# Optimization experiments

Hardware: AMD Instinct MI355X
Metric: run time of the kernel (lower is better)

The kernel has to match this reference:

```python
import jax, jax.numpy as jnp
import numpy as np

N = 100000      # nodes
E = 1000000     # edges
H_DIM = 124     # node embedding dim
CLS_DIM = 4     # node class-logit dim (H_DIM + CLS_DIM = in_features = 128)
POLAR_DIM = 2   # edge_pred_features
HIDDEN = 256
OUT = 2
LN_EPS = 1e-5


def setup_inputs() -> dict:
    key = jax.random.key(0)
    ks = jax.random.split(key, 10)
    in_dim = 2 * (H_DIM + CLS_DIM) + POLAR_DIM  # 258
    return {
        "h": jax.random.normal(ks[0], (N, H_DIM), dtype=jnp.float32),
        "cls": jax.random.normal(ks[1], (N, CLS_DIM), dtype=jnp.float32),
        "polar": jax.random.normal(ks[2], (E, POLAR_DIM), dtype=jnp.float32),
        "src": jax.random.randint(ks[3], (E,), 0, N, dtype=jnp.int64),
        "dst": jax.random.randint(ks[4], (E,), 0, N, dtype=jnp.int64),
        # parameters (PyTorch Linear default-ish init scale)
        "W1": jax.random.normal(ks[5], (in_dim, HIDDEN), dtype=jnp.float32) * (1.0 / np.sqrt(in_dim)),
        "b1": jnp.zeros((HIDDEN,), dtype=jnp.float32),
        "gamma": jnp.ones((HIDDEN,), dtype=jnp.float32),
        "beta": jnp.zeros((HIDDEN,), dtype=jnp.float32),
        "W2": jax.random.normal(ks[6], (HIDDEN, OUT), dtype=jnp.float32) * (1.0 / np.sqrt(HIDDEN)),
        "b2": jnp.zeros((OUT,), dtype=jnp.float32),
    }


def reference(h, cls, polar, src, dst, W1, b1, gamma, beta, W2, b2):
    # softmax over class logits per node (same math as softmax on gathered
    # edge copies, but computed once per node)
    cls_sm = jax.nn.softmax(cls, axis=1)                  # [N, CLS_DIM]
    # gather src/dst node features along edges
    x = jnp.concatenate(
        [h[src], cls_sm[src], polar, h[dst], cls_sm[dst]], axis=1
    )                                                     # [E, 258]
    z = x @ W1 + b1                                        # [E, HIDDEN]
    # LayerNorm
    mu = jnp.mean(z, axis=-1, keepdims=True)
    var = jnp.mean(jnp.square(z - mu), axis=-1, keepdims=True)
    z = (z - mu) * jax.lax.rsqrt(var + LN_EPS) * gamma + beta
    z = jax.nn.relu(z)
    # dropout is identity in eval mode
    score = z @ W2 + b2                                    # [E, OUT]
    return score
```

## Files before the change

### kernel.cpp

```cpp
#include <hip/hip_runtime.h>
#include <hip/hip_bf16.h>

#define NN 100000
#define EE 1000000
#define H_DIM 124
#define PCOLS 512
#define LDK 136
#define CW 132

typedef float f32x4 __attribute__((ext_vector_type(4)));
typedef short bf16x8 __attribute__((ext_vector_type(8)));
typedef _Float16 h2 __attribute__((ext_vector_type(2)));

__device__ __forceinline__ unsigned short f2bf(float f) {
    unsigned int x = __float_as_uint(f);
    unsigned int r = (x + 0x7FFFu + ((x >> 16) & 1u)) >> 16;
    return (unsigned short)r;
}
__device__ __forceinline__ unsigned int pk2bf(float a, float b) {
    return (unsigned int)f2bf(a) | ((unsigned int)f2bf(b) << 16);
}
__device__ __forceinline__ unsigned int pk2h(float a, float b) {
    h2 v = (h2){(_Float16)a, (_Float16)b};
    return __builtin_bit_cast(unsigned int, v);
}

__device__ __forceinline__ float fdot2(h2 a, h2 b, float c) {
#if __has_builtin(__builtin_amdgcn_fdot2)
    return __builtin_amdgcn_fdot2(a, b, c, false);
#else
    return c + (float)a[0] * (float)b[0] + (float)a[1] * (float)b[1];
#endif
}

struct alignas(16) H8 { h2 p[4]; };

__global__ __launch_bounds__(256) void build_w1t(const float* __restrict__ W1,
                                                 unsigned short* __restrict__ W1T) {
    int t2 = blockIdx.x * 256 + threadIdx.x;
    int j = t2 >> 7, k = t2 & 127;
    int row = (j < 256) ? k : (130 + k);
    int col = (j < 256) ? j : (j - 256);
    W1T[t2] = f2bf(W1[row * 256 + col]);
}

__global__ __launch_bounds__(256) void p_gemm(const float* __restrict__ h,
                                              const float* __restrict__ cls,
                                              const unsigned short* __restrict__ W1T,
                                              _Float16* __restrict__ P) {
    __shared__ alignas(16) unsigned short As[64 * LDK];
    __shared__ alignas(16) unsigned short Bs[128 * LDK];
    float* Cs = (float*)&Bs[0];
    const int m0 = blockIdx.x * 64;
    const int t = threadIdx.x;

    #pragma unroll
    for (int it = 0; it < 4; ++it) {
        int chunk = t + it * 256;
        int r = chunk >> 4, c8 = chunk & 15;
        int row = m0 + r;
        unsigned int w0 = 0, w1 = 0, w2 = 0, w3 = 0;
        if (row < NN) {
            if (c8 < 15) {
                const float* hp = h + (size_t)row * H_DIM + c8 * 8;
                float4 v0 = *(const float4*)(hp);
                float4 v1 = *(const float4*)(hp + 4);
                w0 = pk2bf(v0.x, v0.y); w1 = pk2bf(v0.z, v0.w);
                w2 = pk2bf(v1.x, v1.y); w3 = pk2bf(v1.z, v1.w);
            } else {
                float4 v0 = *(const float4*)(h + (size_t)row * H_DIM + 120);
                float4 c = *(const float4*)(cls + (size_t)row * 4);
                float m = fmaxf(fmaxf(c.x, c.y), fmaxf(c.z, c.w));
                float e0 = __expf(c.x - m), e1 = __expf(c.y - m);
                float e2 = __expf(c.z - m), e3 = __expf(c.w - m);
                float inv = 1.0f / (e0 + e1 + e2 + e3);
                w0 = pk2bf(v0.x, v0.y); w1 = pk2bf(v0.z, v0.w);
                w2 = pk2bf(e0 * inv, e1 * inv); w3 = pk2bf(e2 * inv, e3 * inv);
            }
        }
        *(uint4*)(&As[r * LDK + c8 * 8]) = make_uint4(w0, w1, w2, w3);
    }
    __syncthreads();

    const int wave = t >> 6, lane = t & 63;
    const int wm = wave & 1, wn = wave >> 1;
    const int lm = lane & 15, quad = lane >> 4;

    bf16x8 afrag[4][2];
    #pragma unroll
    for (int s = 0; s < 4; ++s) {
        int k0 = s * 32 + quad * 8;
        #pragma unroll
        for (int mt = 0; mt < 2; ++mt)
            afrag[s][mt] = *(const bf16x8*)(&As[(wm * 32 + mt * 16 + lm) * LDK + k0]);
    }

    for (int cchunk = 0; cchunk < 4; ++cchunk) {
        const int n0 = cchunk * 128;
        if (cchunk) __syncthreads();
        #pragma unroll
        for (int it = 0; it < 8; ++it) {
            int chunk = t + it * 256;
            int r = chunk >> 4, c = chunk & 15;
            float4 v = *(const float4*)(W1T + (n0 + r) * 128 + c * 8);
            *(float4*)(&Bs[r * LDK + c * 8]) = v;
        }
        __syncthreads();

        f32x4 acc[2][4];
        #pragma unroll
        for (int mt = 0; mt < 2; ++mt)
            #pragma unroll
            for (int nt = 0; nt < 4; ++nt)
                acc[mt][nt] = (f32x4){0.f, 0.f, 0.f, 0.f};

        #pragma unroll
        for (int s = 0; s < 4; ++s) {
            int k0 = s * 32 + quad * 8;
            bf16x8 b[4];
            #pragma unroll
            for (int nt = 0; nt < 4; ++nt)
                b[nt] = *(const bf16x8*)(&Bs[(wn * 64 + nt * 16 + lm) * LDK + k0]);
            #pragma unroll
            for (int mt = 0; mt < 2; ++mt)
                #pragma unroll
                for (int nt = 0; nt < 4; ++nt)
                    acc[mt][nt] = __builtin_amdgcn_mfma_f32_16x16x32_bf16(afrag[s][mt], b[nt], acc[mt][nt], 0, 0, 0);
        }
        __syncthreads();

        #pragma unroll
        for (int mt = 0; mt < 2; ++mt)
            #pragma unroll
            for (int nt = 0; nt < 4; ++nt) {
                int col = wn * 64 + nt * 16 + lm;
                int rb  = wm * 32 + mt * 16 + quad * 4;
                #pragma unroll
                for (int r = 0; r < 4; ++r)
                    Cs[(rb + r) * CW + col] = acc[mt][nt][r];
            }
        __syncthreads();

        #pragma unroll
        for (int it = 0; it < 4; ++it) {
            int chunk = t + it * 256;
            int r = chunk >> 4, c8 = chunk & 15;
            float4 a = *(const float4*)(Cs + r * CW + c8 * 8);
            float4 b = *(const float4*)(Cs + r * CW + c8 * 8 + 4);
            uint4 o = make_uint4(pk2h(a.x, a.y), pk2h(a.z, a.w),
                                 pk2h(b.x, b.y), pk2h(b.z, b.w));
            int row = m0 + r;
            if (row < NN)
                *(uint4*)(P + (size_t)row * PCOLS + n0 + c8 * 8) = o;
        }
    }
}

#define K3_BLOCKS 2048
#define K3_WAVES (K3_BLOCKS * 4)

__global__ __launch_bounds__(256) void edge_kernel(const _Float16* __restrict__ P,
                                                   const int* __restrict__ src,
                                                   const int* __restrict__ dst,
                                                   const float* __restrict__ polar,
                                                   const float* __restrict__ W1,
                                                   const float* __restrict__ b1,
                                                   const float* __restrict__ gamma,
                                                   const float* __restrict__ beta,
                                                   const float* __restrict__ W2,
                                                   const float* __restrict__ b2,
                                                   float* __restrict__ out) {
    const int lane = threadIdx.x & 63;
    const int il   = lane & 31;
    const int half = lane >> 5;
    const int wid  = blockIdx.x * 4 + (threadIdx.x >> 6);
    const int jb   = il * 8;

    h2 w0c[4], w1c[4], b1c[4], gc[4], bc[4], w2ac[4], w2bc[4];
    #pragma unroll
    for (int p = 0; p < 4; ++p) {
        int j = jb + 2 * p;
        float2 a0 = *(const float2*)(W1 + 128 * 256 + j);
        float2 a1 = *(const float2*)(W1 + 129 * 256 + j);
        float2 ab = *(const float2*)(b1 + j);
        float2 ag = *(const float2*)(gamma + j);
        float2 ae = *(const float2*)(beta + j);
        float4 w2v = *(const float4*)(W2 + 2 * j);
        w0c[p]  = (h2){(_Float16)a0.x, (_Float16)a0.y};
        w1c[p]  = (h2){(_Float16)a1.x, (_Float16)a1.y};
        b1c[p]  = (h2){(_Float16)ab.x, (_Float16)ab.y};
        gc[p]   = (h2){(_Float16)ag.x, (_Float16)ag.y};
        bc[p]   = (h2){(_Float16)ae.x, (_Float16)ae.y};
        w2ac[p] = (h2){(_Float16)w2v.x, (_Float16)w2v.z};
        w2bc[p] = (h2){(_Float16)w2v.y, (_Float16)w2v.w};
    }
    const float b20 = b2[0], b21 = b2[1];
    const h2 onep = (h2){(_Float16)1.0f, (_Float16)1.0f};
    const h2 zerop = (h2){(_Float16)0.0f, (_Float16)0.0f};

    const int stride = K3_WAVES * 2;
    const int base = wid * 2;

    int s0, d0, s1, d1;
    float q00, q01, q10, q11;
    {
        int b = base, e = (b < EE) ? (b + half) : 0;
        s0 = src[e]; d0 = dst[e];
        float2 pw = *(const float2*)(polar + 2 * e);
        q00 = pw.x; q01 = pw.y;
    }
    {
        int b = base + stride, e = (b < EE) ? (b + half) : 0;
        s1 = src[e]; d1 = dst[e];
        float2 pw = *(const float2*)(polar + 2 * e);
        q10 = pw.x; q11 = pw.y;
    }
    H8 ps = *(const H8*)(P + (size_t)s0 * PCOLS + jb);
    H8 pd = *(const H8*)(P + (size_t)d0 * PCOLS + 256 + jb);

    for (int e = base; e < EE; e += stride) {
        int s2, d2; float q20, q21;
        {
            int b = e + 2 * stride, ec = (b < EE) ? (b + half) : 0;
            s2 = src[ec]; d2 = dst[ec];
            float2 pw = *(const float2*)(polar + 2 * ec);
            q20 = pw.x; q21 = pw.y;
        }
        H8 psn = *(const H8*)(P + (size_t)s1 * PCOLS + jb);
        H8 pdn = *(const H8*)(P + (size_t)d1 * PCOLS + 256 + jb);

        h2 p0h = (h2){(_Float16)q00, (_Float16)q00};
        h2 p1h = (h2){(_Float16)q01, (_Float16)q01};
        h2 z[4];
        float sum = 0.f, ss = 0.f;
        #pragma unroll
        for (int p = 0; p < 4; ++p) {
            h2 c = w0c[p] * p0h + (w1c[p] * p1h + b1c[p]);
            z[p] = (ps.p[p] + pd.p[p]) + c;
            sum = fdot2(z[p], onep, sum);
            ss  = fdot2(z[p], z[p], ss);
        }
        #pragma unroll
        for (int off = 16; off; off >>= 1) {
            sum += __shfl_xor(sum, off);
            ss  += __shfl_xor(ss, off);
        }
        float mu   = sum * (1.0f / 256.0f);
        float var  = ss * (1.0f / 256.0f) - mu * mu;
        float rstd = rsqrtf(var + 1e-5f);
        h2 muh = (h2){(_Float16)mu, (_Float16)mu};
        h2 rsh = (h2){(_Float16)rstd, (_Float16)rstd};

        float o0 = 0.f, o1 = 0.f;
        #pragma unroll
        for (int p = 0; p < 4; ++p) {
            h2 t = (z[p] - muh) * rsh;
            h2 u = t * gc[p] + bc[p];
            u = __builtin_elementwise_max(u, zerop);
            o0 = fdot2(u, w2ac[p], o0);
            o1 = fdot2(u, w2bc[p], o1);
        }
        #pragma unroll
        for (int off = 16; off; off >>= 1) {
            o0 += __shfl_xor(o0, off);
            o1 += __shfl_xor(o1, off);
        }
        if (il == 0) {
            *(float2*)(out + 2 * (e + half)) = make_float2(o0 + b20, o1 + b21);
        }

        s0 = s1; d0 = d1; q00 = q10; q01 = q11;
        s1 = s2; d1 = d2; q10 = q20; q11 = q21;
        ps = psn; pd = pdn;
    }
}

extern "C" void kernel_launch(void* const* d_in, const int* in_sizes, int n_in,
                              void* d_out, int out_size, void* d_ws, size_t ws_size,
                              hipStream_t stream) {
    const float* h     = (const float*)d_in[0];
    const float* cls   = (const float*)d_in[1];
    const float* polar = (const float*)d_in[2];
    const int*   src   = (const int*)d_in[3];
    const int*   dst   = (const int*)d_in[4];
    const float* W1    = (const float*)d_in[5];
    const float* b1    = (const float*)d_in[6];
    const float* gamma = (const float*)d_in[7];
    const float* beta  = (const float*)d_in[8];
    const float* W2    = (const float*)d_in[9];
    const float* b2    = (const float*)d_in[10];
    float* out = (float*)d_out;

    char* ws = (char*)d_ws;
    _Float16*       P   = (_Float16*)ws;
    unsigned short* W1T = (unsigned short*)(ws + 102400000);

    build_w1t<<<256, 256, 0, stream>>>(W1, W1T);

    p_gemm<<<1563, 256, 0, stream>>>(h, cls, W1T, P);

    edge_kernel<<<K3_BLOCKS, 256, 0, stream>>>(P, src, dst, polar, W1, b1, gamma, beta, W2, b2, out);
}
```

Baseline: 303.1 us.

## Process four edges per wave with 16-lane groups, DPP reductions, fold b1 into P

The edge kernel now gives each edge 16 lanes with 16 hidden columns apiece, so a wave handles four edges at once instead of two. Each wave runs a fixed 16-round fully unrolled loop over a doubled grid, double-buffering the index and P gathers. The cross-lane sums for LayerNorm and the output dot product use DPP row operations in place of shuffles. Bias b1 is added once per node in the P GEMM epilogue rather than per edge. This cuts shuffle latency and per-edge arithmetic and gives wider per-lane loads, at the cost of more registers per lane and a launch geometry hard-coded to cover exactly E edges.

```diff
diff --git a/kernel.cpp b/kernel.cpp
--- a/kernel.cpp
+++ b/kernel.cpp
@@ -32,6 +32,28 @@
     return c + (float)a[0] * (float)b[0] + (float)a[1] * (float)b[1];
 #endif
 }
+
+#if __has_builtin(__builtin_amdgcn_update_dpp)
+template <int CTRL>
+__device__ __forceinline__ float dpp_add(float x) {
+    int xi = __builtin_bit_cast(int, x);
+    int t = __builtin_amdgcn_update_dpp(xi, xi, CTRL, 0xF, 0xF, false);
+    return x + __builtin_bit_cast(float, t);
+}
+__device__ __forceinline__ float reduce16(float x) {
+    x = dpp_add<0x128>(x);
+    x = dpp_add<0x124>(x);
+    x = dpp_add<0x122>(x);
+    x = dpp_add<0x121>(x);
+    return x;
+}
+#else
+__device__ __forceinline__ float reduce16(float x) {
+    x += __shfl_xor(x, 8); x += __shfl_xor(x, 4);
+    x += __shfl_xor(x, 2); x += __shfl_xor(x, 1);
+    return x;
+}
+#endif
 
 struct alignas(16) H8 { h2 p[4]; };
 
@@ -47,6 +69,7 @@
 __global__ __launch_bounds__(256) void p_gemm(const float* __restrict__ h,
                                               const float* __restrict__ cls,
                                               const unsigned short* __restrict__ W1T,
+                                              const float* __restrict__ b1,
                                               _Float16* __restrict__ P) {
     __shared__ alignas(16) unsigned short As[64 * LDK];
     __shared__ alignas(16) unsigned short Bs[128 * LDK];
@@ -147,6 +170,13 @@
             int r = chunk >> 4, c8 = chunk & 15;
             float4 a = *(const float4*)(Cs + r * CW + c8 * 8);
             float4 b = *(const float4*)(Cs + r * CW + c8 * 8 + 4);
+            if (n0 >= 256) {
+                int cb = n0 + c8 * 8 - 256;
+                float4 ba = *(const float4*)(b1 + cb);
+                float4 bb = *(const float4*)(b1 + cb + 4);
+                a.x += ba.x; a.y += ba.y; a.z += ba.z; a.w += ba.w;
+                b.x += bb.x; b.y += bb.y; b.z += bb.z; b.w += bb.w;
+            }
             uint4 o = make_uint4(pk2h(a.x, a.y), pk2h(a.z, a.w),
                                  pk2h(b.x, b.y), pk2h(b.z, b.w));
             int row = m0 + r;
@@ -156,123 +186,126 @@
     }
 }
 
-#define K3_BLOCKS 2048
-#define K3_WAVES (K3_BLOCKS * 4)
+#define K3_BLOCKS 4096
+#define K3_WAVES  (K3_BLOCKS * 4)
+#define K3_STRIDE (K3_WAVES * 4)
+#define K3_ROUNDS 16
+
+struct EIdx { int s, d; float q0, q1; };
+
+__device__ __forceinline__ EIdx load_idx(int eg, const int* __restrict__ src,
+                                         const int* __restrict__ dst,
+                                         const float* __restrict__ polar) {
+    int ec = (eg < EE) ? eg : 0;
+    EIdx r;
+    r.s = src[ec]; r.d = dst[ec];
+    float2 q = *(const float2*)(polar + 2 * ec);
+    r.q0 = q.x; r.q1 = q.y;
+    return r;
+}
+
+__device__ __forceinline__ void load_p(const _Float16* __restrict__ P, const EIdx& I,
+                                       int il, H8* A) {
+    const _Float16* ps = P + (size_t)I.s * PCOLS + il * 16;
+    A[0] = *(const H8*)(ps);
+    A[1] = *(const H8*)(ps + 8);
+    const _Float16* pd = P + (size_t)I.d * PCOLS + 256 + il * 16;
+    A[2] = *(const H8*)(pd);
+    A[3] = *(const H8*)(pd + 8);
+}
 
 __global__ __launch_bounds__(256) void edge_kernel(const _Float16* __restrict__ P,
                                                    const int* __restrict__ src,
                                                    const int* __restrict__ dst,
                                                    const float* __restrict__ polar,
                                                    const float* __restrict__ W1,
-                                                   const float* __restrict__ b1,
                                                    const float* __restrict__ gamma,
                                                    const float* __restrict__ beta,
                                                    const float* __restrict__ W2,
                                                    const float* __restrict__ b2,
                                                    float* __restrict__ out) {
     const int lane = threadIdx.x & 63;
-    const int il   = lane & 31;
-    const int half = lane >> 5;
+    const int il   = lane & 15;
+    const int g    = lane >> 4;
     const int wid  = blockIdx.x * 4 + (threadIdx.x >> 6);
-    const int jb   = il * 8;
-
-    h2 w0c[4], w1c[4], b1c[4], gc[4], bc[4], w2ac[4], w2bc[4];
+    const int jb   = il * 16;
+
+    h2 w0c[8], w1c[8], gc[8], bc[8], w2ac[8], w2bc[8];
     #pragma unroll
-    for (int p = 0; p < 4; ++p) {
+    for (int p = 0; p < 8; ++p) {
         int j = jb + 2 * p;
         float2 a0 = *(const float2*)(W1 + 128 * 256 + j);
         float2 a1 = *(const float2*)(W1 + 129 * 256 + j);
-        float2 ab = *(const float2*)(b1 + j);
         float2 ag = *(const float2*)(gamma + j);
         float2 ae = *(const float2*)(beta + j);
         float4 w2v = *(const float4*)(W2 + 2 * j);
         w0c[p]  = (h2){(_Float16)a0.x, (_Float16)a0.y};
         w1c[p]  = (h2){(_Float16)a1.x, (_Float16)a1.y};
-        b1c[p]  = (h2){(_Float16)ab.x, (_Float16)ab.y};
         gc[p]   = (h2){(_Float16)ag.x, (_Float16)ag.y};
         bc[p]   = (h2){(_Float16)ae.x, (_Float16)ae.y};
         w2ac[p] = (h2){(_Float16)w2v.x, (_Float16)w2v.z};
         w2bc[p] = (h2){(_Float16)w2v.y, (_Float16)w2v.w};
     }
     const float b20 = b2[0], b21 = b2[1];
-    const h2 onep = (h2){(_Float16)1.0f, (_Float16)1.0f};
+    const h2 onep  = (h2){(_Float16)1.0f, (_Float16)1.0f};
     const h2 zerop = (h2){(_Float16)0.0f, (_Float16)0.0f};
 
-    const int stride = K3_WAVES * 2;
-    const int base = wid * 2;
-
-    int s0, d0, s1, d1;
-    float q00, q01, q10, q11;
-    {
-        int b = base, e = (b < EE) ? (b + half) : 0;
-        s0 = src[e]; d0 = dst[e];
-        float2 pw = *(const float2*)(polar + 2 * e);
-        q00 = pw.x; q01 = pw.y;
-    }
-    {
-        int b = base + stride, e = (b < EE) ? (b + half) : 0;
-        s1 = src[e]; d1 = dst[e];
-        float2 pw = *(const float2*)(polar + 2 * e);
-        q10 = pw.x; q11 = pw.y;
-    }
-    H8 ps = *(const H8*)(P + (size_t)s0 * PCOLS + jb);
-    H8 pd = *(const H8*)(P + (size_t)d0 * PCOLS + 256 + jb);
-
-    for (int e = base; e < EE; e += stride) {
-        int s2, d2; float q20, q21;
-        {
-            int b = e + 2 * stride, ec = (b < EE) ? (b + half) : 0;
-            s2 = src[ec]; d2 = dst[ec];
-            float2 pw = *(const float2*)(polar + 2 * ec);
-            q20 = pw.x; q21 = pw.y;
-        }
-        H8 psn = *(const H8*)(P + (size_t)s1 * PCOLS + jb);
-        H8 pdn = *(const H8*)(P + (size_t)d1 * PCOLS + 256 + jb);
-
-        h2 p0h = (h2){(_Float16)q00, (_Float16)q00};
-        h2 p1h = (h2){(_Float16)q01, (_Float16)q01};
-        h2 z[4];
-        float sum = 0.f, ss = 0.f;
-        #pragma unroll
-        for (int p = 0; p < 4; ++p) {
-            h2 c = w0c[p] * p0h + (w1c[p] * p1h + b1c[p]);
-            z[p] = (ps.p[p] + pd.p[p]) + c;
-            sum = fdot2(z[p], onep, sum);
-            ss  = fdot2(z[p], z[p], ss);
-        }
-        #pragma unroll
-        for (int off = 16; off; off >>= 1) {
-            sum += __shfl_xor(sum, off);
-            ss  += __shfl_xor(ss, off);
-        }
-        float mu   = sum * (1.0f / 256.0f);
-        float var  = ss * (1.0f / 256.0f) - mu * mu;
-        float rstd = rsqrtf(var + 1e-5f);
-        h2 muh = (h2){(_Float16)mu, (_Float16)mu};
-        h2 rsh = (h2){(_Float16)rstd, (_Float16)rstd};
-
-        float o0 = 0.f, o1 = 0.f;
-        #pragma unroll
-        for (int p = 0; p < 4; ++p) {
-            h2 t = (z[p] - muh) * rsh;
-            h2 u = t * gc[p] + bc[p];
-            u = __builtin_elementwise_max(u, zerop);
-            o0 = fdot2(u, w2ac[p], o0);
-            o1 = fdot2(u, w2bc[p], o1);
-        }
-        #pragma unroll
-        for (int off = 16; off; off >>= 1) {
-            o0 += __shfl_xor(o0, off);
-            o1 += __shfl_xor(o1, off);
-        }
-        if (il == 0) {
-            *(float2*)(out + 2 * (e + half)) = make_float2(o0 + b20, o1 + b21);
-        }
-
-        s0 = s1; d0 = d1; q00 = q10; q01 = q11;
-        s1 = s2; d1 = d2; q10 = q20; q11 = q21;
-        ps = psn; pd = pdn;
-    }
+    const int e0 = wid * 4 + g;
+
+    EIdx I0 = load_idx(e0, src, dst, polar);
+    H8 A[4]; load_p(P, I0, il, A);
+    EIdx I1 = load_idx(e0 + K3_STRIDE, src, dst, polar);
+    H8 B[4]; load_p(P, I1, il, B);
+
+    #define EDGE_COMPUTE(Abuf, Ix, eg)                                        \
+    {                                                                          \
+        h2 p0 = (h2){(_Float16)(Ix).q0, (_Float16)(Ix).q0};                    \
+        h2 p1 = (h2){(_Float16)(Ix).q1, (_Float16)(Ix).q1};                    \
+        h2 z[8];                                                               \
+        float sum = 0.f, ss = 0.f;                                             \
+        _Pragma("unroll")                                                      \
+        for (int p = 0; p < 8; ++p) {                                          \
+            h2 pv = ((p < 4) ? (Abuf)[0].p[p] : (Abuf)[1].p[p - 4])            \
+                  + ((p < 4) ? (Abuf)[2].p[p] : (Abuf)[3].p[p - 4]);           \
+            h2 c = w0c[p] * p0 + w1c[p] * p1;                                  \
+            z[p] = pv + c;                                                     \
+            sum = fdot2(z[p], onep, sum);                                      \
+            ss  = fdot2(z[p], z[p], ss);                                       \
+        }                                                                      \
+        sum = reduce16(sum); ss = reduce16(ss);                                \
+        float mu   = sum * (1.0f / 256.0f);                                    \
+        float var  = ss * (1.0f / 256.0f) - mu * mu;                           \
+        float rstd = rsqrtf(var + 1e-5f);                                      \
+        h2 muh = (h2){(_Float16)mu, (_Float16)mu};                             \
+        h2 rsh = (h2){(_Float16)rstd, (_Float16)rstd};                         \
+        float o0 = 0.f, o1 = 0.f;                                              \
+        _Pragma("unroll")                                                      \
+        for (int p = 0; p < 8; ++p) {                                          \
+            h2 tt = (z[p] - muh) * rsh;                                        \
+            h2 u = tt * gc[p] + bc[p];                                         \
+            u = __builtin_elementwise_max(u, zerop);                           \
+            o0 = fdot2(u, w2ac[p], o0);                                        \
+            o1 = fdot2(u, w2bc[p], o1);                                        \
+        }                                                                      \
+        o0 = reduce16(o0); o1 = reduce16(o1);                                  \
+        if (il == 0 && (eg) < EE)                                              \
+            *(float2*)(out + 2 * (eg)) = make_float2(o0 + b20, o1 + b21);      \
+    }
+
+    #pragma unroll
+    for (int r = 0; r < K3_ROUNDS; r += 2) {
+        EDGE_COMPUTE(A, I0, e0 + r * K3_STRIDE);
+        if (r + 2 < K3_ROUNDS) {
+            I0 = load_idx(e0 + (r + 2) * K3_STRIDE, src, dst, polar);
+            load_p(P, I0, il, A);
+        }
+        EDGE_COMPUTE(B, I1, e0 + (r + 1) * K3_STRIDE);
+        if (r + 3 < K3_ROUNDS) {
+            I1 = load_idx(e0 + (r + 3) * K3_STRIDE, src, dst, polar);
+            load_p(P, I1, il, B);
+        }
+    }
+    #undef EDGE_COMPUTE
 }
 
 extern "C" void kernel_launch(void* const* d_in, const int* in_sizes, int n_in,
@@ -296,8 +329,6 @@
     unsigned short* W1T = (unsigned short*)(ws + 102400000);
 
     build_w1t<<<256, 256, 0, stream>>>(W1, W1T);
-
-    p_gemm<<<1563, 256, 0, stream>>>(h, cls, W1T, P);
-
-    edge_kernel<<<K3_BLOCKS, 256, 0, stream>>>(P, src, dst, polar, W1, b1, gamma, beta, W2, b2, out);
-}
+    p_gemm<<<1563, 256, 0, stream>>>(h, cls, W1T, b1, P);
+    edge_kernel<<<K3_BLOCKS, 256, 0, stream>>>(P, src, dst, polar, W1, gamma, beta, W2, b2, out);
+}
```

New measurement: 292.7 us. -3.4%, faster.
